# Optimization experiments

Measured on AMD Instinct MI355X. Metric: run time of the kernel, lower is better.

Reference implementation:

```python
import jax, jax.numpy as jnp
import numpy as np

EPSILON = 1e-7  # wl-coref utils.add_dummy epsilon
LEAKY_SLOPE = 0.01  # torch.nn.LeakyReLU default

N_MENTIONS = 10000
BATCH = 512
N_ANTS = 50
MENTION_EMB = 1024
PW_EMB = 64
IN_FEATURES = 3 * MENTION_EMB + PW_EMB  # 3136
HIDDEN = 128


def setup_inputs() -> dict:
    key = jax.random.key(0)
    ks = jax.random.split(key, 9)
    return {
        "all_mentions": jax.random.normal(ks[0], (N_MENTIONS, MENTION_EMB), jnp.float32),
        "mentions_batch": jax.random.normal(ks[1], (BATCH, MENTION_EMB), jnp.float32),
        "pw_batch": jax.random.normal(ks[2], (BATCH, N_ANTS, PW_EMB), jnp.float32),
        "top_indices_batch": jax.random.randint(ks[3], (BATCH, N_ANTS), 0, N_MENTIONS, jnp.int64 if jax.config.jax_enable_x64 else jnp.int32),
        "top_rough_scores_batch": jax.random.normal(ks[4], (BATCH, N_ANTS), jnp.float32),
        "W1": jax.random.normal(ks[5], (IN_FEATURES, HIDDEN), jnp.float32) * 0.02,
        "b1": jax.random.normal(ks[6], (HIDDEN,), jnp.float32) * 0.02,
        "W_out": jax.random.normal(ks[7], (HIDDEN, 1), jnp.float32) * 0.02,
        "b_out": jax.random.normal(ks[8], (1,), jnp.float32) * 0.02,
    }


def reference(all_mentions, mentions_batch, pw_batch, top_indices_batch,
              top_rough_scores_batch, W1, b1, W_out, b_out):
    batch, n_ants = top_indices_batch.shape
    emb = mentions_batch.shape[1]
    # pair matrix: [batch, n_ants, 3*emb + pw_emb]
    a_mentions = jnp.broadcast_to(mentions_batch[:, None, :], (batch, n_ants, emb))
    b_mentions = all_mentions[top_indices_batch]          # gather: [batch, n_ants, emb]
    similarity = a_mentions * b_mentions
    pair_matrix = jnp.concatenate((a_mentions, b_mentions, similarity, pw_batch), axis=2)
    # FFNN: Linear -> LeakyReLU -> (Dropout=identity in eval) -> Linear(out=1)
    h = jax.nn.leaky_relu(jnp.einsum('baf,fh->bah', pair_matrix, W1) + b1, LEAKY_SLOPE)
    ffnn = (jnp.einsum('bah,ho->bao', h, W_out) + b_out)[..., 0]  # [batch, n_ants]
    scores = top_rough_scores_batch + ffnn
    # add_dummy(eps=True): prepend a column of EPSILON
    dummy = jnp.full((batch, 1), EPSILON, dtype=scores.dtype)
    return jnp.concatenate((dummy, scores), axis=1)  # [batch, n_ants + 1]
```

## Files before the change

kernel.cpp:

```cpp
#include <hip/hip_runtime.h>

#define N_MENT   10000
#define BATCH    512
#define N_ANTS   50
#define EMB      1024
#define PW_EMB   64
#define IN_F     3136
#define HID      128
#define M_TOT    (BATCH * N_ANTS)
#define EPS_VAL  1e-7f
#define SLOPE    0.01f

#define NKT      98
#define CONV_BLK 196
#define MAIN_BLK (M_TOT / 32)

using f32x4 = __attribute__((ext_vector_type(4))) float;
using s16x8 = __attribute__((ext_vector_type(8))) short;
using u16x4 = __attribute__((ext_vector_type(4))) unsigned short;
using u16x8 = __attribute__((ext_vector_type(8))) unsigned short;

__device__ __forceinline__ unsigned short f2bf(float f) {
  unsigned u = __builtin_bit_cast(unsigned, f);
  u += 0x7FFFu + ((u >> 16) & 1u);
  return (unsigned short)(u >> 16);
}

__device__ __forceinline__ u16x4 pack4(float4 v) {
  union { u16x4 o; unsigned u[2]; } r;
  asm("v_cvt_pk_bf16_f32 %0, %1, %2" : "=v"(r.u[0]) : "v"(v.x), "v"(v.y));
  asm("v_cvt_pk_bf16_f32 %0, %1, %2" : "=v"(r.u[1]) : "v"(v.z), "v"(v.w));
  return r.o;
}

__device__ __forceinline__ float4 fmul4(float4 a, float4 b) {
  return make_float4(a.x * b.x, a.y * b.y, a.z * b.z, a.w * b.w);
}

__device__ __forceinline__ int tile_orig_k(int tk) {
  if (tk >= 96) return 3072 + (tk - 96) * 32;
  const int c = tk / 6, r = tk % 6;
  return (r >> 1) * 1024 + c * 64 + (r & 1) * 32;
}

__global__ __launch_bounds__(256) void k_convert(const float* __restrict__ w1,
                                                 unsigned short* __restrict__ w1f) {
  const int id   = blockIdx.x * 256 + threadIdx.x;
  const int lane = id & 63;
  const int tile = id >> 6;
  const int tk   = tile % NKT, tn = tile / NKT;
  const int n    = tn * 16 + (lane & 15);
  const int k    = tile_orig_k(tk) + (lane >> 4) * 8;
  u16x8 o;
  #pragma unroll
  for (int j = 0; j < 8; ++j) o[j] = f2bf(w1[(size_t)(k + j) * HID + n]);
  *(u16x8*)(w1f + (size_t)id * 8) = o;
}

__global__ __launch_bounds__(512) void k_main(
    const float* __restrict__ all_m, const float* __restrict__ men,
    const float* __restrict__ pw, const int* __restrict__ topi,
    const float* __restrict__ rough, const unsigned short* __restrict__ w1f,
    const float* __restrict__ b1, const float* __restrict__ wout,
    const float* __restrict__ bout, float* __restrict__ out) {
  __shared__ __align__(16) unsigned short Xs[2][3][32 * 72];
  __shared__ float red[8 * 32];

  const int t  = threadIdx.x;
  const int m0 = blockIdx.x * 32;

  const int sr = t >> 4, sq = t & 15;
  const int m  = m0 + sr;
  const int bb = m / N_ANTS;
  const int bidx = topi[m];
  const float* pA = men   + (size_t)bb   * EMB    + sq * 4;
  const float* pB = all_m + (size_t)bidx * EMB    + sq * 4;
  const float* pP = pw    + (size_t)m    * PW_EMB + sq * 4;

  const int lane = t & 63, wid = t >> 6;
  const int ln = lane & 15, lg = lane >> 4;
  const unsigned short* wf = w1f + (size_t)wid * NKT * 512 + lane * 8;

  f32x4 acc[2] = {};

  float4 av = ((const float4*)pA)[0];
  float4 bv = ((const float4*)pB)[0];

  int buf = 0;
  for (int c = 0; c < 16; ++c) {
    *(u16x4*)&Xs[buf][0][sr * 72 + sq * 4] = pack4(av);
    *(u16x4*)&Xs[buf][1][sr * 72 + sq * 4] = pack4(bv);
    *(u16x4*)&Xs[buf][2][sr * 72 + sq * 4] = pack4(fmul4(av, bv));

    if (c < 15) {
      av = ((const float4*)(pA + (c + 1) * 64))[0];
      bv = ((const float4*)(pB + (c + 1) * 64))[0];
    } else {
      av = ((const float4*)pP)[0];
    }

    s16x8 wr[6];
    #pragma unroll
    for (int j = 0; j < 6; ++j)
      wr[j] = *(const s16x8*)(wf + (size_t)(c * 6 + j) * 512);

    __syncthreads();
    #pragma unroll
    for (int j = 0; j < 6; ++j) {
      const int reg = j >> 1, ks = j & 1;
      s16x8 x0 = *(const s16x8*)&Xs[buf][reg][ln * 72        + ks * 32 + lg * 8];
      s16x8 x1 = *(const s16x8*)&Xs[buf][reg][(16 + ln) * 72 + ks * 32 + lg * 8];
      acc[0] = __builtin_amdgcn_mfma_f32_16x16x32_bf16(x0, wr[j], acc[0], 0, 0, 0);
      acc[1] = __builtin_amdgcn_mfma_f32_16x16x32_bf16(x1, wr[j], acc[1], 0, 0, 0);
    }
    buf ^= 1;
  }

  {
    *(u16x4*)&Xs[buf][0][sr * 72 + sq * 4] = pack4(av);
    s16x8 wr[2];
    #pragma unroll
    for (int ks = 0; ks < 2; ++ks)
      wr[ks] = *(const s16x8*)(wf + (size_t)(96 + ks) * 512);
    __syncthreads();
    #pragma unroll
    for (int ks = 0; ks < 2; ++ks) {
      s16x8 x0 = *(const s16x8*)&Xs[buf][0][ln * 72        + ks * 32 + lg * 8];
      s16x8 x1 = *(const s16x8*)&Xs[buf][0][(16 + ln) * 72 + ks * 32 + lg * 8];
      acc[0] = __builtin_amdgcn_mfma_f32_16x16x32_bf16(x0, wr[ks], acc[0], 0, 0, 0);
      acc[1] = __builtin_amdgcn_mfma_f32_16x16x32_bf16(x1, wr[ks], acc[1], 0, 0, 0);
    }
  }

  const int n0 = wid * 16 + ln;
  const float bias = b1[n0], w_o = wout[n0];
  #pragma unroll
  for (int mf = 0; mf < 2; ++mf)
    #pragma unroll
    for (int e = 0; e < 4; ++e) {
      float h = acc[mf][e] + bias;
      h = h > 0.f ? h : SLOPE * h;
      float ss = h * w_o;
      ss += __shfl_xor(ss, 1);
      ss += __shfl_xor(ss, 2);
      ss += __shfl_xor(ss, 4);
      ss += __shfl_xor(ss, 8);
      if (ln == 0) red[wid * 32 + mf * 16 + lg * 4 + e] = ss;
    }
  __syncthreads();
  if (t < 32) {
    const int gm = m0 + t;
    float v = red[t];
    #pragma unroll
    for (int w = 1; w < 8; ++w) v += red[w * 32 + t];
    const int gb = gm / N_ANTS;
    const int ga = gm - gb * N_ANTS;
    out[(size_t)gb * (N_ANTS + 1) + 1 + ga] = rough[gm] + v + bout[0];
  }
  if (t == 0) {
    for (int g = m0 / N_ANTS; g <= (m0 + 31) / N_ANTS; ++g)
      out[(size_t)g * (N_ANTS + 1)] = EPS_VAL;
  }
}

__global__ void k_eps(float* __restrict__ out) {
  out[(size_t)threadIdx.x * (N_ANTS + 1)] = EPS_VAL;
}

__global__ __launch_bounds__(128) void k_fb(const float* __restrict__ all_m,
                                            const float* __restrict__ men,
                                            const float* __restrict__ pw,
                                            const int*   __restrict__ topi,
                                            const float* __restrict__ rough,
                                            const float* __restrict__ w1,
                                            const float* __restrict__ b1,
                                            const float* __restrict__ wout,
                                            const float* __restrict__ bout,
                                            float* __restrict__ out) {
  __shared__ float xs[IN_F];
  __shared__ float hred[HID];
  const int pair = blockIdx.x;
  const int t = threadIdx.x;
  const int bb = pair / N_ANTS;
  const int idx = topi[pair];
  const float* pA = men + (size_t)bb * EMB;
  const float* pB = all_m + (size_t)idx * EMB;
  for (int k = t; k < EMB; k += 128) {
    float a = pA[k], b = pB[k];
    xs[k] = a; xs[EMB + k] = b; xs[2 * EMB + k] = a * b;
  }
  if (t < PW_EMB) xs[3 * EMB + t] = pw[(size_t)pair * PW_EMB + t];
  __syncthreads();
  float acc = 0.f;
  for (int k = 0; k < IN_F; ++k) acc = fmaf(xs[k], w1[(size_t)k * HID + t], acc);
  acc += b1[t];
  acc = acc > 0.f ? acc : SLOPE * acc;
  hred[t] = acc * wout[t];
  __syncthreads();
  for (int off = 64; off > 0; off >>= 1) {
    if (t < off) hred[t] += hred[t + off];
    __syncthreads();
  }
  if (t == 0)
    out[(size_t)bb * (N_ANTS + 1) + 1 + (pair - bb * N_ANTS)] = rough[pair] + hred[0] + bout[0];
}

extern "C" void kernel_launch(void* const* d_in, const int* in_sizes, int n_in,
                              void* d_out, int out_size, void* d_ws, size_t ws_size,
                              hipStream_t stream) {
  const float* all_m = (const float*)d_in[0];
  const float* men   = (const float*)d_in[1];
  const float* pw    = (const float*)d_in[2];
  const int*   topi  = (const int*)  d_in[3];
  const float* rough = (const float*)d_in[4];
  const float* w1    = (const float*)d_in[5];
  const float* b1    = (const float*)d_in[6];
  const float* wout  = (const float*)d_in[7];
  const float* bout  = (const float*)d_in[8];
  float* out = (float*)d_out;

  const size_t W1F_BYTES = (size_t)HID * IN_F * sizeof(unsigned short);

  if (ws_size >= W1F_BYTES) {
    unsigned short* w1f = (unsigned short*)d_ws;
    k_convert<<<CONV_BLK, 256, 0, stream>>>(w1, w1f);
    k_main<<<MAIN_BLK, 512, 0, stream>>>(all_m, men, pw, topi, rough, w1f,
                                         b1, wout, bout, out);
  } else {
    k_eps<<<1, BATCH, 0, stream>>>(out);
    k_fb<<<M_TOT, 128, 0, stream>>>(all_m, men, pw, topi, rough, w1, b1, wout, bout, out);
  }
}
```

Measured before the change: 54.30 us.

## Double block M-tile to 64 rows and prefetch next W1 k-chunk into registers

Each block now handles 64 pair rows instead of 32, with each thread staging 8 elements per row and each wave issuing four MFMAs per weight fragment, so every W1 load is reused across twice as many rows and total weight traffic halves. The weight fragments for the next k-chunk are loaded into a second register set while the current chunk's MFMAs run, overlapping global latency with compute. In exchange the grid halves to 400 blocks, LDS use doubles and register pressure rises, which may reduce occupancy and leave the GPU's compute units underfilled.

```diff
diff --git a/kernel.cpp b/kernel.cpp
--- a/kernel.cpp
+++ b/kernel.cpp
@@ -13,7 +13,7 @@
 
 #define NKT      98
 #define CONV_BLK 196
-#define MAIN_BLK (M_TOT / 32)
+#define MAIN_BLK (M_TOT / 64)
 
 using f32x4 = __attribute__((ext_vector_type(4))) float;
 using s16x8 = __attribute__((ext_vector_type(8))) short;
@@ -63,102 +63,113 @@
     const float* __restrict__ rough, const unsigned short* __restrict__ w1f,
     const float* __restrict__ b1, const float* __restrict__ wout,
     const float* __restrict__ bout, float* __restrict__ out) {
-  __shared__ __align__(16) unsigned short Xs[2][3][32 * 72];
-  __shared__ float red[8 * 32];
+  __shared__ __align__(16) unsigned short Xs[2][3][64 * 72];
+  __shared__ float red[8][64];
 
   const int t  = threadIdx.x;
-  const int m0 = blockIdx.x * 32;
-
-  const int sr = t >> 4, sq = t & 15;
+  const int m0 = blockIdx.x * 64;
+
+  const int sr = t >> 3, sq = t & 7;
   const int m  = m0 + sr;
   const int bb = m / N_ANTS;
   const int bidx = topi[m];
-  const float* pA = men   + (size_t)bb   * EMB    + sq * 4;
-  const float* pB = all_m + (size_t)bidx * EMB    + sq * 4;
-  const float* pP = pw    + (size_t)m    * PW_EMB + sq * 4;
+  const float* pA = men   + (size_t)bb   * EMB    + sq * 8;
+  const float* pB = all_m + (size_t)bidx * EMB    + sq * 8;
+  const float* pP = pw    + (size_t)m    * PW_EMB + sq * 8;
 
   const int lane = t & 63, wid = t >> 6;
   const int ln = lane & 15, lg = lane >> 4;
   const unsigned short* wf = w1f + (size_t)wid * NKT * 512 + lane * 8;
 
-  f32x4 acc[2] = {};
-
-  float4 av = ((const float4*)pA)[0];
-  float4 bv = ((const float4*)pB)[0];
+  f32x4 acc[4] = {};
+
+  float4 av0 = ((const float4*)pA)[0], av1 = ((const float4*)pA)[1];
+  float4 bv0 = ((const float4*)pB)[0], bv1 = ((const float4*)pB)[1];
+
+  s16x8 wcur[6], wnext[6];
+  #pragma unroll
+  for (int j = 0; j < 6; ++j)
+    wcur[j] = *(const s16x8*)(wf + (size_t)j * 512);
 
   int buf = 0;
   for (int c = 0; c < 16; ++c) {
-    *(u16x4*)&Xs[buf][0][sr * 72 + sq * 4] = pack4(av);
-    *(u16x4*)&Xs[buf][1][sr * 72 + sq * 4] = pack4(bv);
-    *(u16x4*)&Xs[buf][2][sr * 72 + sq * 4] = pack4(fmul4(av, bv));
+    *(u16x4*)&Xs[buf][0][sr * 72 + sq * 8]     = pack4(av0);
+    *(u16x4*)&Xs[buf][0][sr * 72 + sq * 8 + 4] = pack4(av1);
+    *(u16x4*)&Xs[buf][1][sr * 72 + sq * 8]     = pack4(bv0);
+    *(u16x4*)&Xs[buf][1][sr * 72 + sq * 8 + 4] = pack4(bv1);
+    *(u16x4*)&Xs[buf][2][sr * 72 + sq * 8]     = pack4(fmul4(av0, bv0));
+    *(u16x4*)&Xs[buf][2][sr * 72 + sq * 8 + 4] = pack4(fmul4(av1, bv1));
 
     if (c < 15) {
-      av = ((const float4*)(pA + (c + 1) * 64))[0];
-      bv = ((const float4*)(pB + (c + 1) * 64))[0];
+      const float* qA = pA + (c + 1) * 64;
+      const float* qB = pB + (c + 1) * 64;
+      av0 = ((const float4*)qA)[0]; av1 = ((const float4*)qA)[1];
+      bv0 = ((const float4*)qB)[0]; bv1 = ((const float4*)qB)[1];
     } else {
-      av = ((const float4*)pP)[0];
-    }
-
-    s16x8 wr[6];
-    #pragma unroll
-    for (int j = 0; j < 6; ++j)
-      wr[j] = *(const s16x8*)(wf + (size_t)(c * 6 + j) * 512);
+      av0 = ((const float4*)pP)[0]; av1 = ((const float4*)pP)[1];
+    }
+
+    #pragma unroll
+    for (int j = 0; j < 6; ++j) {
+      const int tkn = (c < 15) ? (c + 1) * 6 + j : (j < 2 ? 96 + j : 97);
+      wnext[j] = *(const s16x8*)(wf + (size_t)tkn * 512);
+    }
 
     __syncthreads();
     #pragma unroll
     for (int j = 0; j < 6; ++j) {
       const int reg = j >> 1, ks = j & 1;
-      s16x8 x0 = *(const s16x8*)&Xs[buf][reg][ln * 72        + ks * 32 + lg * 8];
-      s16x8 x1 = *(const s16x8*)&Xs[buf][reg][(16 + ln) * 72 + ks * 32 + lg * 8];
-      acc[0] = __builtin_amdgcn_mfma_f32_16x16x32_bf16(x0, wr[j], acc[0], 0, 0, 0);
-      acc[1] = __builtin_amdgcn_mfma_f32_16x16x32_bf16(x1, wr[j], acc[1], 0, 0, 0);
-    }
+      #pragma unroll
+      for (int mt = 0; mt < 4; ++mt) {
+        s16x8 x = *(const s16x8*)&Xs[buf][reg][(mt * 16 + ln) * 72 + ks * 32 + lg * 8];
+        acc[mt] = __builtin_amdgcn_mfma_f32_16x16x32_bf16(x, wcur[j], acc[mt], 0, 0, 0);
+      }
+    }
+    #pragma unroll
+    for (int j = 0; j < 6; ++j) wcur[j] = wnext[j];
     buf ^= 1;
   }
 
   {
-    *(u16x4*)&Xs[buf][0][sr * 72 + sq * 4] = pack4(av);
-    s16x8 wr[2];
+    *(u16x4*)&Xs[buf][0][sr * 72 + sq * 8]     = pack4(av0);
+    *(u16x4*)&Xs[buf][0][sr * 72 + sq * 8 + 4] = pack4(av1);
+    __syncthreads();
     #pragma unroll
     for (int ks = 0; ks < 2; ++ks)
-      wr[ks] = *(const s16x8*)(wf + (size_t)(96 + ks) * 512);
-    __syncthreads();
-    #pragma unroll
-    for (int ks = 0; ks < 2; ++ks) {
-      s16x8 x0 = *(const s16x8*)&Xs[buf][0][ln * 72        + ks * 32 + lg * 8];
-      s16x8 x1 = *(const s16x8*)&Xs[buf][0][(16 + ln) * 72 + ks * 32 + lg * 8];
-      acc[0] = __builtin_amdgcn_mfma_f32_16x16x32_bf16(x0, wr[ks], acc[0], 0, 0, 0);
-      acc[1] = __builtin_amdgcn_mfma_f32_16x16x32_bf16(x1, wr[ks], acc[1], 0, 0, 0);
-    }
+      #pragma unroll
+      for (int mt = 0; mt < 4; ++mt) {
+        s16x8 x = *(const s16x8*)&Xs[buf][0][(mt * 16 + ln) * 72 + ks * 32 + lg * 8];
+        acc[mt] = __builtin_amdgcn_mfma_f32_16x16x32_bf16(x, wcur[ks], acc[mt], 0, 0, 0);
+      }
   }
 
   const int n0 = wid * 16 + ln;
   const float bias = b1[n0], w_o = wout[n0];
   #pragma unroll
-  for (int mf = 0; mf < 2; ++mf)
+  for (int mt = 0; mt < 4; ++mt)
     #pragma unroll
     for (int e = 0; e < 4; ++e) {
-      float h = acc[mf][e] + bias;
+      float h = acc[mt][e] + bias;
       h = h > 0.f ? h : SLOPE * h;
       float ss = h * w_o;
       ss += __shfl_xor(ss, 1);
       ss += __shfl_xor(ss, 2);
       ss += __shfl_xor(ss, 4);
       ss += __shfl_xor(ss, 8);
-      if (ln == 0) red[wid * 32 + mf * 16 + lg * 4 + e] = ss;
+      if (ln == 0) red[wid][mt * 16 + lg * 4 + e] = ss;
     }
   __syncthreads();
-  if (t < 32) {
+  if (t < 64) {
     const int gm = m0 + t;
-    float v = red[t];
-    #pragma unroll
-    for (int w = 1; w < 8; ++w) v += red[w * 32 + t];
+    float v = red[0][t];
+    #pragma unroll
+    for (int w = 1; w < 8; ++w) v += red[w][t];
     const int gb = gm / N_ANTS;
     const int ga = gm - gb * N_ANTS;
     out[(size_t)gb * (N_ANTS + 1) + 1 + ga] = rough[gm] + v + bout[0];
   }
   if (t == 0) {
-    for (int g = m0 / N_ANTS; g <= (m0 + 31) / N_ANTS; ++g)
+    for (int g = m0 / N_ANTS; g <= (m0 + 63) / N_ANTS; ++g)
       out[(size_t)g * (N_ANTS + 1)] = EPS_VAL;
   }
 }
```

New measurement: 49.22 us. 9.4% less time.
